# Kernel optimization log

Hardware: AMD Instinct MI355X
Metric: run time of the kernel (lower is better)

## Reference

```python
import jax, jax.numpy as jnp
import numpy as np

N = 100000
E = 1600000
IN_F = 128
OUT_F = 64
NEG_SLOPE = 0.2


def setup_inputs() -> dict:
    key = jax.random.key(0)
    k1, k2, k3, k4 = jax.random.split(key, 4)
    h = jax.random.normal(k1, (N, IN_F), dtype=jnp.float32)
    edge_index = jax.random.randint(k2, (2, E), 0, N, dtype=jnp.int64 if jax.config.jax_enable_x64 else jnp.int32)
    # glorot-initialized params (scale ~ sqrt(6/(fan_in+fan_out)))
    ws = float(np.sqrt(6.0 / (IN_F + OUT_F)))
    W = jax.random.uniform(k3, (OUT_F, IN_F), dtype=jnp.float32, minval=-ws, maxval=ws)
    as_ = float(np.sqrt(6.0 / (1 + 2 * OUT_F)))
    a = jax.random.uniform(k4, (1, 2 * OUT_F), dtype=jnp.float32, minval=-as_, maxval=as_)
    return {"h": h, "W": W, "a": a, "edge_index": edge_index}


def reference(h, W, a, edge_index):
    n = h.shape[0]
    f_out = W.shape[0]
    h_lin = h @ W.T  # [N, F_out]
    # add self loops
    loops = jnp.arange(n, dtype=edge_index.dtype)
    row = jnp.concatenate([edge_index[0], loops])  # [E+N]
    col = jnp.concatenate([edge_index[1], loops])
    # cat([h_lin[row], h_lin[col]]) @ a.T == h_lin[row]@a1 + h_lin[col]@a2
    a1 = a[0, :f_out]
    a2 = a[0, f_out:]
    s_src = h_lin @ a1  # [N]
    s_dst = h_lin @ a2  # [N]
    e = s_src[row] + s_dst[col]  # [E+N]
    e = jnp.where(e > 0, e, NEG_SLOPE * e)  # LeakyReLU
    # segment softmax over destination (row); every row appears via self loop
    m = jax.ops.segment_max(e, row, num_segments=n)
    ex = jnp.exp(e - m[row])
    denom = jax.ops.segment_sum(ex, row, num_segments=n)
    alpha = ex / denom[row]
    # scatter-add aggregation
    h_prime = jax.ops.segment_sum(alpha[:, None] * h_lin[col], row, num_segments=n)
    return jax.nn.elu(h_prime)
```

## Files before the change

### kernel.cpp

```cpp
#include <hip/hip_runtime.h>
#include <cstdint>

#define N_NODES 100000
#define E_EDGES 1600000
#define TOTAL_E (E_EDGES + N_NODES)
#define IN_F 128
#define OUT_F 64
#define NEG_SLOPE 0.2f

#define NB   256
#define RPB  391
#define GCAP 8192
#define TILE 4096
#define EPT  (TILE / 256)
#define HALF_R 196
#define CCAP 4608

typedef __attribute__((ext_vector_type(8))) short short8;
typedef __attribute__((ext_vector_type(4))) float float4v;

__device__ __forceinline__ short bf16_rne(float x) {
  unsigned u = __builtin_bit_cast(unsigned, x);
  unsigned r = u + 0x7FFFu + ((u >> 16) & 1u);
  return (short)(r >> 16);
}
__device__ __forceinline__ float bf16_f(short s) {
  unsigned u = ((unsigned)(unsigned short)s) << 16;
  return __builtin_bit_cast(float, u);
}

__global__ __launch_bounds__(256) void k_linear(
    const float* __restrict__ h, const float* __restrict__ W,
    const float* __restrict__ a, unsigned short* __restrict__ h_lin,
    float* __restrict__ s_src, float* __restrict__ s_dst) {
  __shared__ alignas(16) short Whi[16 * 512];
  __shared__ alignas(16) short Wlo[16 * 512];

  const int tid = threadIdx.x;
  for (int i = tid; i < OUT_F * IN_F; i += 256) {
    const int n = i >> 7, k = i & 127;
    const float x = W[i];
    const short hi = bf16_rne(x);
    const short lo = bf16_rne(x - bf16_f(hi));
    const int idx = (((k >> 5) * 4 + (n >> 4)) << 9) |
                    (((((k >> 3) & 3) << 4) | (n & 15)) << 3) | (k & 7);
    Whi[idx] = hi;
    Wlo[idx] = lo;
  }
  __syncthreads();

  const int lane = tid & 63;
  const int m    = lane & 15;
  const int q    = lane >> 4;
  const int wgid = blockIdx.x * 4 + (tid >> 6);
  const int nw   = gridDim.x * 4;

  float a1v[4], a2v[4];
#pragma unroll
  for (int t = 0; t < 4; ++t) {
    a1v[t] = a[t * 16 + m];
    a2v[t] = a[OUT_F + t * 16 + m];
  }

  for (int tile = wgid; tile < N_NODES / 16; tile += nw) {
    const int row0 = tile * 16;
    float4v acc[4] = {{0.f,0.f,0.f,0.f},{0.f,0.f,0.f,0.f},
                      {0.f,0.f,0.f,0.f},{0.f,0.f,0.f,0.f}};

    const float* hbase = h + (size_t)(row0 + m) * IN_F + q * 8;
#pragma unroll
    for (int ks = 0; ks < 4; ++ks) {
      const float4 f0 = *(const float4*)(hbase + 32 * ks);
      const float4 f1 = *(const float4*)(hbase + 32 * ks + 4);
      float av[8] = {f0.x, f0.y, f0.z, f0.w, f1.x, f1.y, f1.z, f1.w};
      short8 ahi, alo;
#pragma unroll
      for (int j = 0; j < 8; ++j) {
        const short hi = bf16_rne(av[j]);
        ahi[j] = hi;
        alo[j] = bf16_rne(av[j] - bf16_f(hi));
      }
#pragma unroll
      for (int t = 0; t < 4; ++t) {
        const int fb = ((ks * 4 + t) << 9) + lane * 8;
        const short8 bhi = *(const short8*)&Whi[fb];
        const short8 blo = *(const short8*)&Wlo[fb];
        acc[t] = __builtin_amdgcn_mfma_f32_16x16x32_bf16(ahi, bhi, acc[t], 0, 0, 0);
        acc[t] = __builtin_amdgcn_mfma_f32_16x16x32_bf16(ahi, blo, acc[t], 0, 0, 0);
        acc[t] = __builtin_amdgcn_mfma_f32_16x16x32_bf16(alo, bhi, acc[t], 0, 0, 0);
      }
    }

#pragma unroll
    for (int t = 0; t < 4; ++t)
#pragma unroll
      for (int r = 0; r < 4; ++r)
        h_lin[(size_t)(row0 + q * 4 + r) * OUT_F + t * 16 + m] =
            (unsigned short)bf16_rne(acc[t][r]);

#pragma unroll
    for (int r = 0; r < 4; ++r) {
      float p = acc[0][r] * a1v[0] + acc[1][r] * a1v[1] +
                acc[2][r] * a1v[2] + acc[3][r] * a1v[3];
      float qq = acc[0][r] * a2v[0] + acc[1][r] * a2v[1] +
                 acc[2][r] * a2v[2] + acc[3][r] * a2v[3];
#pragma unroll
      for (int o = 1; o < 16; o <<= 1) {
        p  += __shfl_xor(p, o, 64);
        qq += __shfl_xor(qq, o, 64);
      }
      if (m == 0) {
        s_src[row0 + q * 4 + r] = p;
        s_dst[row0 + q * 4 + r] = qq;
      }
    }
  }
}

__global__ __launch_bounds__(256) void k_bin(
    const int* __restrict__ ei, int* __restrict__ gcur,
    unsigned* __restrict__ regions) {
  __shared__ unsigned reord[TILE];
  __shared__ unsigned char bktid[TILE];
  __shared__ int hist[NB];
  __shared__ int scan_s[NB];
  __shared__ int adj[NB];
  __shared__ int wsum[4];

  const int tid = threadIdx.x;
  const int e0  = blockIdx.x * TILE;

  hist[tid] = 0;
  __syncthreads();

  int      myb[EPT];
  unsigned myrec[EPT];
#pragma unroll
  for (int k = 0; k < EPT; ++k) {
    const int e = e0 + k * 256 + tid;
    int b = -1; unsigned rec = 0;
    if (e < TOTAL_E) {
      int r, c;
      if (e < E_EDGES) { r = ei[e]; c = ei[E_EDGES + e]; }
      else             { r = e - E_EDGES; c = r; }
      b = (int)((unsigned)r / RPB);
      rec = ((unsigned)(r - b * RPB) << 17) | (unsigned)c;
      atomicAdd(&hist[b], 1);
    }
    myb[k] = b; myrec[k] = rec;
  }
  __syncthreads();

  const int lane = tid & 63, w = tid >> 6;
  {
    const int v = hist[tid];
    int incl = v;
#pragma unroll
    for (int o = 1; o < 64; o <<= 1) {
      const int t = __shfl_up(incl, o, 64);
      if (lane >= o) incl += t;
    }
    if (lane == 63) wsum[w] = incl;
    __syncthreads();
    int wpre = 0;
    for (int i = 0; i < w; ++i) wpre += wsum[i];
    scan_s[tid] = wpre + incl - v;
    adj[tid]    = wpre + incl - v;
  }
  __syncthreads();

#pragma unroll
  for (int k = 0; k < EPT; ++k) {
    if (myb[k] >= 0) {
      const int pos = atomicAdd(&adj[myb[k]], 1);
      reord[pos]  = myrec[k];
      bktid[pos]  = (unsigned char)myb[k];
    }
  }
  __syncthreads();

  {
    const int cnt = hist[tid];
    int a2 = 0;
    if (cnt > 0) a2 = atomicAdd(&gcur[tid], cnt) - scan_s[tid];
    __syncthreads();
    adj[tid] = a2;
  }
  __syncthreads();

  const int tilesz = scan_s[NB - 1] + hist[NB - 1];
  for (int i = tid; i < tilesz; i += 256) {
    const int b    = bktid[i];
    const int slot = adj[b] + i;
    if (slot < GCAP) regions[(size_t)b * GCAP + slot] = reord[i];
  }
}

__global__ __launch_bounds__(1024) void k_agg(
    const unsigned short* __restrict__ h_lin, const float* __restrict__ s_src,
    const float* __restrict__ s_dst, const int* __restrict__ gcur,
    const unsigned* __restrict__ regions, float* __restrict__ out) {
  __shared__ int   cnt[HALF_R];
  __shared__ int   off[HALF_R];
  __shared__ float srcs[HALF_R];
  __shared__ uint2 pairs[CCAP];
  __shared__ int   wsum4[4];

  const int blk  = blockIdx.x;
  const int b    = blk >> 1;
  const int half = blk & 1;
  const int rlo  = half * HALF_R;
  const int hr   = half ? (RPB - HALF_R) : HALF_R;
  const int tid  = threadIdx.x;
  const int row0 = b * RPB + rlo;
  const int m    = min(gcur[b], GCAP);
  const unsigned* reg = regions + (size_t)b * GCAP;

  for (int i = tid; i < HALF_R; i += 1024) {
    cnt[i]  = 0;
    srcs[i] = (i < hr && row0 + i < N_NODES) ? s_src[row0 + i] : 0.f;
  }
  __syncthreads();

  for (int i = tid; i < m; i += 1024) {
    const int rl = (int)(reg[i] >> 17) - rlo;
    if (rl >= 0 && rl < hr) atomicAdd(&cnt[rl], 1);
  }
  __syncthreads();

  const int lane = tid & 63, wv = tid >> 6;
  int incl = 0, v = 0;
  if (tid < 256) {
    v = (tid < hr) ? cnt[tid] : 0;
    incl = v;
#pragma unroll
    for (int o = 1; o < 64; o <<= 1) {
      const int t = __shfl_up(incl, o, 64);
      if (lane >= o) incl += t;
    }
    if (lane == 63) wsum4[wv] = incl;
  }
  __syncthreads();
  if (tid < hr) {
    int wpre = 0;
    for (int i = 0; i < wv; ++i) wpre += wsum4[i];
    off[tid] = wpre + incl - v;
  }
  __syncthreads();

  for (int i = tid; i < m; i += 1024) {
    const unsigned rec = reg[i];
    const int rl = (int)(rec >> 17) - rlo;
    if (rl >= 0 && rl < hr) {
      const int c = (int)(rec & 0x1FFFFu);
      float e = srcs[rl] + s_dst[c];
      e = e > 0.f ? e : NEG_SLOPE * e;
      const float ex = __expf(e);
      const int pos = atomicAdd(&off[rl], 1);
      if (pos < CCAP) pairs[pos] = make_uint2((unsigned)c, __float_as_uint(ex));
    }
  }
  __syncthreads();

  const int hid = lane >> 5;
  const int fl  = (lane & 31) * 2;
  for (int rl = wv; rl < hr; rl += 16) {
    const int row = row0 + rl;
    if (row >= N_NODES) break;
    const int dcnt  = cnt[rl];
    const int end   = off[rl];
    const int start = end - dcnt;

    float accx = 0.f, accy = 0.f, dsum = 0.f;
    int j = hid;
    for (; j + 2 < dcnt; j += 4) {
      const uint2 p0 = pairs[start + j];
      const uint2 p1 = pairs[start + j + 2];
      const unsigned h0 = *(const unsigned*)&h_lin[(size_t)p0.x * OUT_F + fl];
      const unsigned h1 = *(const unsigned*)&h_lin[(size_t)p1.x * OUT_F + fl];
      const float e0 = __uint_as_float(p0.y);
      const float e1 = __uint_as_float(p1.y);
      accx = fmaf(e0, __builtin_bit_cast(float, h0 << 16), accx);
      accy = fmaf(e0, __builtin_bit_cast(float, h0 & 0xFFFF0000u), accy);
      accx = fmaf(e1, __builtin_bit_cast(float, h1 << 16), accx);
      accy = fmaf(e1, __builtin_bit_cast(float, h1 & 0xFFFF0000u), accy);
      dsum += e0 + e1;
    }
    if (j < dcnt) {
      const uint2 p0 = pairs[start + j];
      const unsigned h0 = *(const unsigned*)&h_lin[(size_t)p0.x * OUT_F + fl];
      const float e0 = __uint_as_float(p0.y);
      accx = fmaf(e0, __builtin_bit_cast(float, h0 << 16), accx);
      accy = fmaf(e0, __builtin_bit_cast(float, h0 & 0xFFFF0000u), accy);
      dsum += e0;
    }

    accx += __shfl_xor(accx, 32, 64);
    accy += __shfl_xor(accy, 32, 64);
    dsum += __shfl_xor(dsum, 32, 64);

    if (lane < 32) {
      float hx = accx / dsum, hy = accy / dsum;
      hx = hx > 0.f ? hx : __expf(hx) - 1.f;
      hy = hy > 0.f ? hy : __expf(hy) - 1.f;
      *(float2*)&out[(size_t)row * OUT_F + fl] = make_float2(hx, hy);
    }
  }
}

extern "C" void kernel_launch(void* const* d_in, const int* in_sizes, int n_in,
                              void* d_out, int out_size, void* d_ws, size_t ws_size,
                              hipStream_t stream) {
  const float* h  = (const float*)d_in[0];
  const float* W  = (const float*)d_in[1];
  const float* a  = (const float*)d_in[2];
  const int*   ei = (const int*)d_in[3];
  float* out = (float*)d_out;

  unsigned short* h_lin = (unsigned short*)d_ws;
  float* s_src = (float*)(h_lin + (size_t)N_NODES * OUT_F);
  float* s_dst = s_src + N_NODES;
  int*   gcur  = (int*)(s_dst + N_NODES);
  unsigned* regions = (unsigned*)(gcur + NB);

  hipMemsetAsync(gcur, 0, NB * sizeof(int), stream);

  k_linear<<<782, 256, 0, stream>>>(h, W, a, h_lin, s_src, s_dst);

  k_bin<<<(TOTAL_E + TILE - 1) / TILE, 256, 0, stream>>>(ei, gcur, regions);

  k_agg<<<NB * 2, 1024, 0, stream>>>(h_lin, s_src, s_dst, gcur, regions, out);
}
```

Measured before the change: 182.9 us.

## Merge linear GEMM and edge binning into one heterogeneous front kernel

Combines the dense projection kernel and the edge-binning kernel into a single launch. Block IDs are split so the first blocks do binning and the rest do the GEMM, with both sharing a 32KB shared-memory buffer. The two independent stages can now run concurrently on the GPU and one launch gap disappears. The GEMM grid is reduced from 782 to 608 blocks. Shared-memory use per block is the maximum of the two stages, which may limit occupancy for the binning blocks.

Result: no change. 181.5 us (-0.7%).

```diff
diff --git a/kernel.cpp b/kernel.cpp
--- a/kernel.cpp
+++ b/kernel.cpp
@@ -16,6 +16,10 @@
 #define HALF_R 196
 #define CCAP 4608
 
+#define BIN_BLOCKS ((TOTAL_E + TILE - 1) / TILE)
+#define GEMM_BLOCKS 608
+#define FRONT_BLOCKS (BIN_BLOCKS + GEMM_BLOCKS)
+
 typedef __attribute__((ext_vector_type(8))) short short8;
 typedef __attribute__((ext_vector_type(4))) float float4v;
 
@@ -29,12 +33,13 @@
   return __builtin_bit_cast(float, u);
 }
 
-__global__ __launch_bounds__(256) void k_linear(
+__device__ __forceinline__ void gemm_body(
+    char* smem, int gbid,
     const float* __restrict__ h, const float* __restrict__ W,
     const float* __restrict__ a, unsigned short* __restrict__ h_lin,
     float* __restrict__ s_src, float* __restrict__ s_dst) {
-  __shared__ alignas(16) short Whi[16 * 512];
-  __shared__ alignas(16) short Wlo[16 * 512];
+  short* Whi = (short*)smem;
+  short* Wlo = (short*)(smem + 16384);
 
   const int tid = threadIdx.x;
   for (int i = tid; i < OUT_F * IN_F; i += 256) {
@@ -52,8 +57,8 @@
   const int lane = tid & 63;
   const int m    = lane & 15;
   const int q    = lane >> 4;
-  const int wgid = blockIdx.x * 4 + (tid >> 6);
-  const int nw   = gridDim.x * 4;
+  const int wgid = gbid * 4 + (tid >> 6);
+  const int nw   = GEMM_BLOCKS * 4;
 
   float a1v[4], a2v[4];
 #pragma unroll
@@ -117,18 +122,19 @@
   }
 }
 
-__global__ __launch_bounds__(256) void k_bin(
+__device__ __forceinline__ void bin_body(
+    char* smem, int bbid,
     const int* __restrict__ ei, int* __restrict__ gcur,
     unsigned* __restrict__ regions) {
-  __shared__ unsigned reord[TILE];
-  __shared__ unsigned char bktid[TILE];
-  __shared__ int hist[NB];
-  __shared__ int scan_s[NB];
-  __shared__ int adj[NB];
-  __shared__ int wsum[4];
+  unsigned*      reord  = (unsigned*)smem;
+  unsigned char* bktid  = (unsigned char*)(smem + 16384);
+  int*           hist   = (int*)(smem + 20480);
+  int*           scan_s = (int*)(smem + 21504);
+  int*           adj    = (int*)(smem + 22528);
+  int*           wsum   = (int*)(smem + 23552);
 
   const int tid = threadIdx.x;
-  const int e0  = blockIdx.x * TILE;
+  const int e0  = bbid * TILE;
 
   hist[tid] = 0;
   __syncthreads();
@@ -193,6 +199,21 @@
     const int b    = bktid[i];
     const int slot = adj[b] + i;
     if (slot < GCAP) regions[(size_t)b * GCAP + slot] = reord[i];
+  }
+}
+
+__global__ __launch_bounds__(256) void k_front(
+    const float* __restrict__ h, const float* __restrict__ W,
+    const float* __restrict__ a, const int* __restrict__ ei,
+    unsigned short* __restrict__ h_lin, float* __restrict__ s_src,
+    float* __restrict__ s_dst, int* __restrict__ gcur,
+    unsigned* __restrict__ regions) {
+  __shared__ alignas(16) char smem[32768];
+  const int bid = blockIdx.x;
+  if (bid < BIN_BLOCKS) {
+    bin_body(smem, bid, ei, gcur, regions);
+  } else {
+    gemm_body(smem, bid - BIN_BLOCKS, h, W, a, h_lin, s_src, s_dst);
   }
 }
 
@@ -325,9 +346,8 @@
 
   hipMemsetAsync(gcur, 0, NB * sizeof(int), stream);
 
-  k_linear<<<782, 256, 0, stream>>>(h, W, a, h_lin, s_src, s_dst);
-
-  k_bin<<<(TOTAL_E + TILE - 1) / TILE, 256, 0, stream>>>(ei, gcur, regions);
+  k_front<<<FRONT_BLOCKS, 256, 0, stream>>>(h, W, a, ei, h_lin, s_src, s_dst,
+                                            gcur, regions);
 
   k_agg<<<NB * 2, 1024, 0, stream>>>(h_lin, s_src, s_dst, gcur, regions, out);
 }
```
